# Kernel optimization log

Hardware: AMD Instinct MI355X
Metric: run time of the kernel (lower is better)

## Reference

```python
import jax, jax.numpy as jnp
import numpy as np

EMBED_DIM = 512
N_HEADS = 8
HEAD_DIM = EMBED_DIM // N_HEADS


def setup_inputs() -> dict:
    key = jax.random.key(0)
    ks = jax.random.split(key, 5)
    B, N, D = 2, 4096, EMBED_DIM
    scale = 1.0 / np.sqrt(D)
    x = jax.random.normal(ks[0], (B, N, D), dtype=jnp.float32)
    W_qkv = jax.random.normal(ks[1], (D, 3 * D), dtype=jnp.float32) * scale
    b_qkv = jnp.zeros((3 * D,), dtype=jnp.float32)
    W_out = jax.random.normal(ks[2], (D, D), dtype=jnp.float32) * scale
    b_out = jnp.zeros((D,), dtype=jnp.float32)
    return {"x": x, "W_qkv": W_qkv, "b_qkv": b_qkv, "W_out": W_out, "b_out": b_out}


def reference(x, W_qkv, b_qkv, W_out, b_out):
    B, N, D = x.shape
    H, Hd = N_HEADS, HEAD_DIM
    qkv = x @ W_qkv + b_qkv                      # [B, N, 3D]
    q, k, v = jnp.split(qkv, 3, axis=-1)
    # [B, N, D] -> [B, H, N, Hd]
    q = q.reshape(B, N, H, Hd).transpose(0, 2, 1, 3)
    k = k.reshape(B, N, H, Hd).transpose(0, 2, 1, 3)
    v = v.reshape(B, N, H, Hd).transpose(0, 2, 1, 3)
    scores = jnp.einsum('bhqd,bhkd->bhqk', q, k) / np.sqrt(Hd)  # [B, H, N, N]
    attn = jax.nn.softmax(scores, axis=-1)
    out = jnp.einsum('bhqk,bhkd->bhqd', attn, v)  # [B, H, N, Hd]
    out = out.transpose(0, 2, 1, 3).reshape(B, N, D)
    return out @ W_out + b_out
```

## Files before the change

### kernel.cpp

```cpp
#include <hip/hip_runtime.h>

typedef __attribute__((ext_vector_type(4))) float f32x4;
typedef __attribute__((ext_vector_type(8))) __bf16 bf16x8;
typedef __attribute__((ext_vector_type(4))) __bf16 bf16x4;
typedef __attribute__((ext_vector_type(4))) short s16x4;

#define DEVI static __device__ __forceinline__

#define LOG2E 1.44269504088896340736f
#define THR 10.0f

DEVI short f2bf(float f) {
  return __builtin_bit_cast(short, (__bf16)f);
}

DEVI void gll16(const short* gsrc, short* ldst) {
  __builtin_amdgcn_global_load_lds(
      (const __attribute__((address_space(1))) unsigned*)gsrc,
      (__attribute__((address_space(3))) unsigned*)ldst, 16, 0, 0);
}

DEVI void stage_gran(const short* g, int ldRow, short* lds, int p, int lane) {
  int q = p + lane;
  int row = q >> 3;
  int k8 = (q & 7) ^ (row & 7);
  gll16(g + (size_t)row * ldRow + k8 * 8, lds + (size_t)p * 8);
}

DEVI bf16x8 frag_ld(const short* base, int lane, int kk) {
  int r = lane & 15;
  int chunk = (kk * 4 + (lane >> 4)) ^ (r & 7);
  return *(const bf16x8*)(base + r * 64 + chunk * 8);
}


__global__ void cvt_k(const float* __restrict__ in, short* __restrict__ out, int n4) {
  int i = blockIdx.x * blockDim.x + threadIdx.x;
  if (i < n4) {
    f32x4 v = *(const f32x4*)(in + (size_t)i * 4);
    s16x4 o;
    #pragma unroll
    for (int j = 0; j < 4; ++j) o[j] = f2bf(v[j]);
    *(s16x4*)(out + (size_t)i * 4) = o;
  }
}

__global__ void tcvt_k(const float* __restrict__ in, short* __restrict__ out, int R, int C) {
  __shared__ float t[32][33];
  const int bx = blockIdx.x * 32;
  const int by = blockIdx.y * 32;
  const int lx = threadIdx.x & 31, ly = threadIdx.x >> 5;
  #pragma unroll
  for (int rr = ly; rr < 32; rr += 8)
    t[rr][lx] = in[(size_t)(by + rr) * C + bx + lx];
  __syncthreads();
  #pragma unroll
  for (int cc = ly; cc < 32; cc += 8)
    out[(size_t)(bx + cc) * R + by + lx] = f2bf(t[lx][cc]);
}


template <int EPI>
__global__ __launch_bounds__(256, 3)
void gemm_k(const short* __restrict__ A, const short* __restrict__ Bt,
            const float* __restrict__ bias, float* __restrict__ outF,
            short* __restrict__ Qb, short* __restrict__ Kb, short* __restrict__ Vtb,
            int M, int N, int K) {
  __shared__ __align__(16) short As[128 * 64];
  __shared__ __align__(16) short Bs[128 * 64];
  const int lane = threadIdx.x & 63;
  const int wid  = threadIdx.x >> 6;
  const int mt = blockIdx.x * 128;
  const int nt = blockIdx.y * 128;
  const int wm = (wid >> 1) * 64;
  const int wn = (wid & 1) * 64;

  f32x4 acc[4][4];
  #pragma unroll
  for (int i = 0; i < 4; ++i)
    #pragma unroll
    for (int j = 0; j < 4; ++j) acc[i][j] = (f32x4){0.f, 0.f, 0.f, 0.f};

  const short* Atile = A + (size_t)mt * K;
  const short* Btile = Bt + (size_t)nt * K;
  const int nkt = K >> 6;

  for (int kt = 0; kt < nkt; ++kt) {
    __syncthreads();
    #pragma unroll
    for (int i = 0; i < 4; ++i) {
      stage_gran(Atile + kt * 64, K, As, (wid * 4 + i) * 64, lane);
      stage_gran(Btile + kt * 64, K, Bs, (wid * 4 + i) * 64, lane);
    }
    __syncthreads();
    #pragma unroll
    for (int kk = 0; kk < 2; ++kk) {
      bf16x8 af[4], bfr[4];
      #pragma unroll
      for (int i = 0; i < 4; ++i) af[i] = frag_ld(As + (wm + i * 16) * 64, lane, kk);
      #pragma unroll
      for (int j = 0; j < 4; ++j) bfr[j] = frag_ld(Bs + (wn + j * 16) * 64, lane, kk);
      #pragma unroll
      for (int i = 0; i < 4; ++i)
        #pragma unroll
        for (int j = 0; j < 4; ++j)
          acc[i][j] = __builtin_amdgcn_mfma_f32_16x16x32_bf16(af[i], bfr[j], acc[i][j], 0, 0, 0);
    }
  }

  const int rbase = (lane >> 4) * 4;
  const int cl = lane & 15;
  #pragma unroll
  for (int i = 0; i < 4; ++i) {
    #pragma unroll
    for (int j = 0; j < 4; ++j) {
      const int col = nt + wn + j * 16 + cl;
      const float bv = bias[col];
      #pragma unroll
      for (int r = 0; r < 4; ++r) {
        const int row = mt + wm + i * 16 + rbase + r;
        float v = acc[i][j][r] + bv;
        if (EPI == 1) {
          outF[(size_t)row * N + col] = v;
        } else {
          const int which = col >> 9;
          const int d = col & 511;
          const int h = d >> 6, hd = d & 63;
          const int b = row >> 12, n = row & 4095;
          const int bh = b * 8 + h;
          if (which == 0)
            Qb[((size_t)bh * 4096 + n) * 64 + hd] = f2bf(v * (0.125f * LOG2E));
          else if (which == 1)
            Kb[((size_t)bh * 4096 + n) * 64 + hd] = f2bf(v);
          else
            Vtb[((size_t)bh * 64 + hd) * 4096 + n] = f2bf(v);
        }
      }
    }
  }
}


__global__ __launch_bounds__(256, 2)
void attn_k(const short* __restrict__ Qb, const short* __restrict__ Kb,
            const short* __restrict__ Vtb, short* __restrict__ AOut) {
  __shared__ __align__(16) short Ks[2][64 * 64];
  __shared__ __align__(16) short Vs[3][64 * 64];
  __shared__ __align__(16) short Ps[4][32 * 64];
  const int lane = threadIdx.x & 63;
  const int wid = threadIdx.x >> 6;
  const int bh = blockIdx.y;
  const int qt = blockIdx.x * 128 + wid * 32;
  const short* Qh = Qb + (size_t)bh * 4096 * 64;
  const short* Kh = Kb + (size_t)bh * 4096 * 64;
  const short* Vh = Vtb + (size_t)bh * 64 * 4096;
  const int cl = lane & 15, g = lane >> 4;

  bf16x8 qf[2][2];
  #pragma unroll
  for (int i = 0; i < 2; ++i)
    #pragma unroll
    for (int kd = 0; kd < 2; ++kd)
      qf[i][kd] = *(const bf16x8*)(Qh + (size_t)(qt + i * 16 + cl) * 64 + kd * 32 + g * 8);

  f32x4 o[2][4];
  f32x4 lacc[2];
  #pragma unroll
  for (int i = 0; i < 2; ++i) {
    lacc[i] = (f32x4){0.f, 0.f, 0.f, 0.f};
    #pragma unroll
    for (int jd = 0; jd < 4; ++jd) o[i][jd] = (f32x4){0.f, 0.f, 0.f, 0.f};
  }
  float m[2] = {-1e30f, -1e30f};

  bf16x8 ones;
  #pragma unroll
  for (int e = 0; e < 8; ++e) ones[e] = (__bf16)1.0f;

  short* P = (short*)Ps[wid];
  int pwo[2][4];
  #pragma unroll
  for (int i = 0; i < 2; ++i)
    #pragma unroll
    for (int j = 0; j < 4; ++j)
      pwo[i][j] = (i * 16 + cl) * 64 + (((j * 2 + (g >> 1)) ^ (cl & 7)) * 8) + (g & 1) * 4;

  auto STAGEK = [&](int b, int kv) {
    #pragma unroll
    for (int t = 0; t < 2; ++t)
      stage_gran(Kh + (size_t)kv * 64, 64, Ks[b], (wid * 2 + t) * 64, lane);
  };
  auto STAGEV = [&](int b, int kv) {
    #pragma unroll
    for (int t = 0; t < 2; ++t)
      stage_gran(Vh + kv, 4096, Vs[b], (wid * 2 + t) * 64, lane);
  };

  STAGEK(0, 0);
  STAGEV(0, 0);
  __syncthreads();

  f32x4 s[2][4];
  int vprev = 2, vcur = 0, vnext = 1;

  for (int i = 0; i <= 64; ++i) {
    const int kcur = i & 1;
    if (i < 63) {
      STAGEK(kcur ^ 1, (i + 1) * 64);
      STAGEV(vnext, (i + 1) * 64);
    }

    if (i > 0) {
      bf16x8 vf[2][4];
      #pragma unroll
      for (int kk = 0; kk < 2; ++kk)
        #pragma unroll
        for (int jd = 0; jd < 4; ++jd)
          vf[kk][jd] = frag_ld(Vs[vprev] + jd * 16 * 64, lane, kk);

      float lmax[2];
      #pragma unroll
      for (int i2 = 0; i2 < 2; ++i2) {
        float a = fmaxf(fmaxf(s[i2][0][0], s[i2][0][1]), fmaxf(s[i2][0][2], s[i2][0][3]));
        float b = fmaxf(fmaxf(s[i2][1][0], s[i2][1][1]), fmaxf(s[i2][1][2], s[i2][1][3]));
        float c = fmaxf(fmaxf(s[i2][2][0], s[i2][2][1]), fmaxf(s[i2][2][2], s[i2][2][3]));
        float d = fmaxf(fmaxf(s[i2][3][0], s[i2][3][1]), fmaxf(s[i2][3][2], s[i2][3][3]));
        lmax[i2] = fmaxf(fmaxf(a, b), fmaxf(c, d));
      }

      if (!__all((lmax[0] <= m[0] + THR) && (lmax[1] <= m[1] + THR))) {
        #pragma unroll
        for (int i2 = 0; i2 < 2; ++i2) {
          float mx = lmax[i2];
          mx = fmaxf(mx, __shfl_xor(mx, 16));
          mx = fmaxf(mx, __shfl_xor(mx, 32));
          float mnew = fmaxf(m[i2], mx);
          float corr = exp2f(m[i2] - mnew);
          m[i2] = mnew;
          float c[4];
          #pragma unroll
          for (int r = 0; r < 4; ++r) c[r] = __shfl(corr, (g << 2) | r);
          #pragma unroll
          for (int jd = 0; jd < 4; ++jd)
            #pragma unroll
            for (int r = 0; r < 4; ++r) o[i2][jd][r] *= c[r];
          #pragma unroll
          for (int r = 0; r < 4; ++r) lacc[i2][r] *= c[r];
        }
      }

      #pragma unroll
      for (int i2 = 0; i2 < 2; ++i2)
        #pragma unroll
        for (int j = 0; j < 4; ++j) {
          bf16x4 pw;
          #pragma unroll
          for (int r = 0; r < 4; ++r) pw[r] = (__bf16)exp2f(s[i2][j][r] - m[i2]);
          *(bf16x4*)(P + pwo[i2][j]) = pw;
        }

      __builtin_amdgcn_s_setprio(1);
      #pragma unroll
      for (int kk = 0; kk < 2; ++kk) {
        bf16x8 pf[2];
        #pragma unroll
        for (int i2 = 0; i2 < 2; ++i2) pf[i2] = frag_ld(P + i2 * 16 * 64, lane, kk);
        #pragma unroll
        for (int i2 = 0; i2 < 2; ++i2)
          lacc[i2] = __builtin_amdgcn_mfma_f32_16x16x32_bf16(pf[i2], ones, lacc[i2], 0, 0, 0);
        #pragma unroll
        for (int i2 = 0; i2 < 2; ++i2)
          #pragma unroll
          for (int jd = 0; jd < 4; ++jd)
            o[i2][jd] = __builtin_amdgcn_mfma_f32_16x16x32_bf16(pf[i2], vf[kk][jd], o[i2][jd], 0, 0, 0);
      }
      __builtin_amdgcn_s_setprio(0);
    }

    if (i < 64) {
      #pragma unroll
      for (int i2 = 0; i2 < 2; ++i2)
        #pragma unroll
        for (int j = 0; j < 4; ++j) s[i2][j] = (f32x4){0.f, 0.f, 0.f, 0.f};
      __builtin_amdgcn_s_setprio(1);
      #pragma unroll
      for (int kd = 0; kd < 2; ++kd) {
        bf16x8 kf[4];
        #pragma unroll
        for (int j = 0; j < 4; ++j) kf[j] = frag_ld(Ks[kcur] + j * 16 * 64, lane, kd);
        #pragma unroll
        for (int i2 = 0; i2 < 2; ++i2)
          #pragma unroll
          for (int j = 0; j < 4; ++j)
            s[i2][j] = __builtin_amdgcn_mfma_f32_16x16x32_bf16(kf[j], qf[i2][kd], s[i2][j], 0, 0, 0);
      }
      __builtin_amdgcn_s_setprio(0);
      __syncthreads();
    }

    const int t = vprev; vprev = vcur; vcur = vnext; vnext = t;
  }

  const int b = bh >> 3, h = bh & 7;
  #pragma unroll
  for (int i = 0; i < 2; ++i) {
    #pragma unroll
    for (int r = 0; r < 4; ++r) {
      const float inv = 1.f / lacc[i][r];
      const int n = qt + i * 16 + g * 4 + r;
      #pragma unroll
      for (int jd = 0; jd < 4; ++jd) {
        const int d = h * 64 + jd * 16 + cl;
        AOut[((size_t)b * 4096 + n) * 512 + d] = f2bf(o[i][jd][r] * inv);
      }
    }
  }
}


extern "C" void kernel_launch(void* const* d_in, const int* in_sizes, int n_in,
                              void* d_out, int out_size, void* d_ws, size_t ws_size,
                              hipStream_t stream) {
  const float* x    = (const float*)d_in[0];
  const float* Wqkv = (const float*)d_in[1];
  const float* bqkv = (const float*)d_in[2];
  const float* Wout = (const float*)d_in[3];
  const float* bout = (const float*)d_in[4];
  float* out = (float*)d_out;

  short* ws   = (short*)d_ws;
  short* xb   = ws;
  short* Wqt  = xb + 8192 * 512;
  short* Wot  = Wqt + 1536 * 512;
  short* Qb   = Wot + 512 * 512;
  short* Kb   = Qb + 16 * 4096 * 64;
  short* Vtb  = Kb + 16 * 4096 * 64;
  short* AOut = Vtb + 16 * 4096 * 64;

  hipLaunchKernelGGL(cvt_k, dim3(8192 * 512 / 4 / 256), dim3(256), 0, stream,
                     x, xb, 8192 * 512 / 4);
  hipLaunchKernelGGL(tcvt_k, dim3(1536 / 32, 512 / 32), dim3(256), 0, stream,
                     Wqkv, Wqt, 512, 1536);
  hipLaunchKernelGGL(tcvt_k, dim3(512 / 32, 512 / 32), dim3(256), 0, stream,
                     Wout, Wot, 512, 512);
  hipLaunchKernelGGL(gemm_k<0>, dim3(8192 / 128, 1536 / 128), dim3(256), 0, stream,
                     xb, Wqt, bqkv, (float*)nullptr, Qb, Kb, Vtb, 8192, 1536, 512);
  hipLaunchKernelGGL(attn_k, dim3(4096 / 128, 16), dim3(256), 0, stream,
                     Qb, Kb, Vtb, AOut);
  hipLaunchKernelGGL(gemm_k<1>, dim3(8192 / 128, 512 / 128), dim3(256), 0, stream,
                     AOut, Wot, bout, out, (short*)nullptr, (short*)nullptr, (short*)nullptr,
                     8192, 512, 512);
}
```

Baseline: 244.7 us.

## Keep softmax probabilities in registers and compute row sums with scalar adds

Removes the per-wave LDS round trip for the probability tile: exp'd scores are packed into bf16 registers and fed directly as the A operand of the PV MFMA. V fragments are re-gathered from LDS with a matching permuted layout. The row-sum MFMA against a ones vector is replaced by per-lane fp32 accumulation plus a final cross-lane reduction. This cuts LDS traffic, LDS footprint and MFMA work, at the cost of more scalar adds and an ad-hoc operand layout that must be exactly consistent.

```diff
diff --git a/kernel.cpp b/kernel.cpp
--- a/kernel.cpp
+++ b/kernel.cpp
@@ -31,6 +31,14 @@
   int r = lane & 15;
   int chunk = (kk * 4 + (lane >> 4)) ^ (r & 7);
   return *(const bf16x8*)(base + r * 64 + chunk * 8);
+}
+
+DEVI bf16x4 v64(const short* base, int row, int cg, int sub) {
+  return *(const bf16x4*)(base + row * 64 + ((cg ^ (row & 7)) << 3) + sub);
+}
+
+DEVI bf16x8 cat(bf16x4 a, bf16x4 b) {
+  return __builtin_shufflevector(a, b, 0, 1, 2, 3, 4, 5, 6, 7);
 }
 
 
@@ -146,7 +154,6 @@
             const short* __restrict__ Vtb, short* __restrict__ AOut) {
   __shared__ __align__(16) short Ks[2][64 * 64];
   __shared__ __align__(16) short Vs[3][64 * 64];
-  __shared__ __align__(16) short Ps[4][32 * 64];
   const int lane = threadIdx.x & 63;
   const int wid = threadIdx.x >> 6;
   const int bh = blockIdx.y;
@@ -164,26 +171,12 @@
       qf[i][kd] = *(const bf16x8*)(Qh + (size_t)(qt + i * 16 + cl) * 64 + kd * 32 + g * 8);
 
   f32x4 o[2][4];
-  f32x4 lacc[2];
-  #pragma unroll
-  for (int i = 0; i < 2; ++i) {
-    lacc[i] = (f32x4){0.f, 0.f, 0.f, 0.f};
+  #pragma unroll
+  for (int i = 0; i < 2; ++i)
     #pragma unroll
     for (int jd = 0; jd < 4; ++jd) o[i][jd] = (f32x4){0.f, 0.f, 0.f, 0.f};
-  }
+  float lsum[2] = {0.f, 0.f};
   float m[2] = {-1e30f, -1e30f};
-
-  bf16x8 ones;
-  #pragma unroll
-  for (int e = 0; e < 8; ++e) ones[e] = (__bf16)1.0f;
-
-  short* P = (short*)Ps[wid];
-  int pwo[2][4];
-  #pragma unroll
-  for (int i = 0; i < 2; ++i)
-    #pragma unroll
-    for (int j = 0; j < 4; ++j)
-      pwo[i][j] = (i * 16 + cl) * 64 + (((j * 2 + (g >> 1)) ^ (cl & 7)) * 8) + (g & 1) * 4;
 
   auto STAGEK = [&](int b, int kv) {
     #pragma unroll
@@ -211,13 +204,6 @@
     }
 
     if (i > 0) {
-      bf16x8 vf[2][4];
-      #pragma unroll
-      for (int kk = 0; kk < 2; ++kk)
-        #pragma unroll
-        for (int jd = 0; jd < 4; ++jd)
-          vf[kk][jd] = frag_ld(Vs[vprev] + jd * 16 * 64, lane, kk);
-
       float lmax[2];
       #pragma unroll
       for (int i2 = 0; i2 < 2; ++i2) {
@@ -237,6 +223,7 @@
           float mnew = fmaxf(m[i2], mx);
           float corr = exp2f(m[i2] - mnew);
           m[i2] = mnew;
+          lsum[i2] *= corr;
           float c[4];
           #pragma unroll
           for (int r = 0; r < 4; ++r) c[r] = __shfl(corr, (g << 2) | r);
@@ -244,35 +231,52 @@
           for (int jd = 0; jd < 4; ++jd)
             #pragma unroll
             for (int r = 0; r < 4; ++r) o[i2][jd][r] *= c[r];
-          #pragma unroll
-          for (int r = 0; r < 4; ++r) lacc[i2][r] *= c[r];
-        }
-      }
-
+        }
+      }
+
+      #pragma unroll
+      for (int i2 = 0; i2 < 2; ++i2) {
+        float rs = 0.f;
+        #pragma unroll
+        for (int j = 0; j < 4; ++j)
+          #pragma unroll
+          for (int r = 0; r < 4; ++r) {
+            float p = exp2f(s[i2][j][r] - m[i2]);
+            s[i2][j][r] = p;
+            rs += p;
+          }
+        lsum[i2] += rs;
+      }
+
+      bf16x4 pb[2][4];
       #pragma unroll
       for (int i2 = 0; i2 < 2; ++i2)
         #pragma unroll
         for (int j = 0; j < 4; ++j) {
-          bf16x4 pw;
-          #pragma unroll
-          for (int r = 0; r < 4; ++r) pw[r] = (__bf16)exp2f(s[i2][j][r] - m[i2]);
-          *(bf16x4*)(P + pwo[i2][j]) = pw;
+          bf16x4 w;
+          #pragma unroll
+          for (int r = 0; r < 4; ++r) w[r] = (__bf16)s[i2][j][r];
+          pb[i2][j] = w;
         }
 
       __builtin_amdgcn_s_setprio(1);
       #pragma unroll
       for (int kk = 0; kk < 2; ++kk) {
-        bf16x8 pf[2];
-        #pragma unroll
-        for (int i2 = 0; i2 < 2; ++i2) pf[i2] = frag_ld(P + i2 * 16 * 64, lane, kk);
-        #pragma unroll
-        for (int i2 = 0; i2 < 2; ++i2)
-          lacc[i2] = __builtin_amdgcn_mfma_f32_16x16x32_bf16(pf[i2], ones, lacc[i2], 0, 0, 0);
-        #pragma unroll
-        for (int i2 = 0; i2 < 2; ++i2)
+        bf16x8 vf[4];
+        #pragma unroll
+        for (int jd = 0; jd < 4; ++jd) {
+          const int row = jd * 16 + cl;
+          const int c0 = 4 * kk + (g >> 1);
+          const int sub = (g & 1) * 4;
+          vf[jd] = cat(v64(Vs[vprev], row, c0, sub), v64(Vs[vprev], row, c0 + 2, sub));
+        }
+        #pragma unroll
+        for (int i2 = 0; i2 < 2; ++i2) {
+          bf16x8 pf = cat(pb[i2][2 * kk], pb[i2][2 * kk + 1]);
           #pragma unroll
           for (int jd = 0; jd < 4; ++jd)
-            o[i2][jd] = __builtin_amdgcn_mfma_f32_16x16x32_bf16(pf[i2], vf[kk][jd], o[i2][jd], 0, 0, 0);
+            o[i2][jd] = __builtin_amdgcn_mfma_f32_16x16x32_bf16(pf, vf[jd], o[i2][jd], 0, 0, 0);
+        }
       }
       __builtin_amdgcn_s_setprio(0);
     }
@@ -302,16 +306,24 @@
   }
 
   const int b = bh >> 3, h = bh & 7;
+  float inv[2];
+  #pragma unroll
+  for (int i2 = 0; i2 < 2; ++i2) {
+    float l = lsum[i2];
+    l += __shfl_xor(l, 16);
+    l += __shfl_xor(l, 32);
+    inv[i2] = 1.f / l;
+  }
   #pragma unroll
   for (int i = 0; i < 2; ++i) {
     #pragma unroll
     for (int r = 0; r < 4; ++r) {
-      const float inv = 1.f / lacc[i][r];
+      const float invr = __shfl(inv[i], (g << 2) | r);
       const int n = qt + i * 16 + g * 4 + r;
       #pragma unroll
       for (int jd = 0; jd < 4; ++jd) {
         const int d = h * 64 + jd * 16 + cl;
-        AOut[((size_t)b * 4096 + n) * 512 + d] = f2bf(o[i][jd][r] * inv);
+        AOut[((size_t)b * 4096 + n) * 512 + d] = f2bf(o[i][jd][r] * invr);
       }
     }
   }
```

Result: no change. 243.8 us (-0.4%).
